# Kernel optimization log

Measured on AMD Instinct MI355X. Metric: run time of the kernel, lower is better.

Reference implementation:

```python
import jax, jax.numpy as jnp
import numpy as np

IN_FEATURES = 128
OUT_FEATURES = 128
GRID_SIZE = 5
SPLINE_ORDER = 3
N_KNOTS = GRID_SIZE + 2 * SPLINE_ORDER + 1  # 12
N_BASIS = GRID_SIZE + SPLINE_ORDER          # 8


def b_spline_basis(x, grid, spline_order):
    # x: [N, in], grid: [in, n_knots] -> basis: [N, in, n_basis]
    xe = x[..., None]
    basis = ((xe >= grid[..., :-1]) & (xe < grid[..., 1:])).astype(x.dtype)
    for k in range(1, spline_order + 1):
        left = (xe - grid[..., :-(k + 1)]) / (grid[..., k:-1] - grid[..., :-(k + 1)] + 1e-08)
        right = (grid[..., k + 1:] - xe) / (grid[..., k + 1:] - grid[..., 1:-k] + 1e-08)
        basis = left * basis[..., :-1] + right * basis[..., 1:]
    return basis


def setup_inputs() -> dict:
    key = jax.random.key(0)
    k_x, k_bw, k_sw = jax.random.split(key, 3)
    x = jax.random.normal(k_x, (16, 4096, IN_FEATURES), dtype=jnp.float32)
    grid = jnp.tile(jnp.linspace(-1.0, 1.0, N_KNOTS, dtype=jnp.float32)[None, :], (IN_FEATURES, 1))
    base_weight = jax.random.normal(k_bw, (OUT_FEATURES, IN_FEATURES), dtype=jnp.float32) * 0.1
    base_bias = jnp.zeros((OUT_FEATURES,), dtype=jnp.float32)
    spline_weight = jax.random.normal(k_sw, (OUT_FEATURES, IN_FEATURES, N_BASIS), dtype=jnp.float32) * 0.1
    spline_bias = jnp.zeros((OUT_FEATURES,), dtype=jnp.float32)
    spline_scale = jnp.ones((1,), dtype=jnp.float32)
    return {"x": x, "grid": grid, "base_weight": base_weight, "base_bias": base_bias,
            "spline_weight": spline_weight, "spline_bias": spline_bias, "spline_scale": spline_scale}


def reference(x, grid, base_weight, base_bias, spline_weight, spline_bias, spline_scale):
    orig_shape = x.shape
    x_flat = x.reshape(-1, IN_FEATURES)                      # [N, in]
    base_out = jax.nn.silu(x_flat) @ base_weight.T + base_bias  # [N, out]
    x_norm = jnp.tanh(x_flat)
    basis = b_spline_basis(x_norm, grid, SPLINE_ORDER)       # [N, in, n_basis]
    spline_out = jnp.einsum('oib,nib->no', spline_weight, basis) + spline_bias
    out = base_out + spline_scale * spline_out
    return out.reshape(*orig_shape[:-1], OUT_FEATURES)
```

## Files before the change

kernel.cpp:

```cpp
#include <hip/hip_runtime.h>
#include <hip/hip_bf16.h>


typedef __attribute__((ext_vector_type(8))) short short8;
typedef __attribute__((ext_vector_type(4))) float f32x4;
typedef __attribute__((ext_vector_type(4))) unsigned int u32x4;
typedef __attribute__((ext_vector_type(8))) unsigned short u16x8;

#define GLOAD_LDS16(g, l) __builtin_amdgcn_global_load_lds(                 \
    (const __attribute__((address_space(1))) void*)(g),                     \
    (__attribute__((address_space(3))) void*)(l), 16, 0, 0)

__device__ __forceinline__ unsigned short f2bf(float f) {
    unsigned u = __builtin_bit_cast(unsigned, f);
    return (unsigned short)((u + 0x7fffu + ((u >> 16) & 1u)) >> 16);
}
__device__ __forceinline__ unsigned pack_bf2(float lo, float hi) {
    unsigned r;
    asm("v_cvt_pk_bf16_f32 %0, %1, %2" : "=v"(r) : "v"(lo), "v"(hi));
    return r;
}
__device__ __forceinline__ float fexp2(float f) { return __builtin_amdgcn_exp2f(f); }
__device__ __forceinline__ float frcp(float f)  { return __builtin_amdgcn_rcpf(f); }
__device__ __forceinline__ float fsilu(float v) {
    return v * frcp(1.0f + fexp2(v * -1.442695041f));
}

__device__ __forceinline__ short8 spline_frag(float xv) {
    const float s6 = 0.16666667f;
    float e  = fexp2(xv * 2.885390082f);
    float r  = frcp(1.0f + e);
    float t  = __builtin_fmaf(-2.0f, r, 1.0f);
    float u  = __builtin_fmaf(t, 5.5f, 5.5f);
    int   j  = (int)u;
    float w  = u - (float)j;
    float w2 = w * w;
    float v0 = __builtin_fmaf(__builtin_fmaf(__builtin_fmaf(-s6, w, 0.5f), w, -0.5f), w, s6);
    float v1 = __builtin_fmaf(__builtin_fmaf(0.5f, w, -1.0f), w2, 0.66666667f);
    float v3 = (w * s6) * w2;
    float v2 = (1.0f - v0) - (v1 + v3);
    unsigned P01 = pack_bf2(v0, v1);
    unsigned P23 = pack_bf2(v2, v3);
    unsigned long long P = (unsigned long long)P01 | ((unsigned long long)P23 << 32);
    int s = (j - 3) << 4;
    unsigned long long lo, hi;
    lo = (s >= 0) ? ((s < 64) ? (P << s) : 0ull) : (P >> (-s));
    hi = (s <= 0) ? 0ull
                  : ((s < 64) ? (P >> (64 - s))
                              : ((s < 128) ? (P << (s - 64)) : 0ull));
    u32x4 f = { (unsigned)lo, (unsigned)(lo >> 32), (unsigned)hi, (unsigned)(hi >> 32) };
    return __builtin_bit_cast(short8, f);
}

__global__ void kan_prep(const float* __restrict__ spline_w,
                         const float* __restrict__ base_w,
                         const float* __restrict__ scale_p,
                         unsigned short* __restrict__ wpre) {
    int g   = blockIdx.x * 256 + threadIdx.x;
    int hp  = g >> 10;
    int rem = g & 1023;
    int o   = rem >> 3;
    int k0  = (rem & 7) << 3;
    const float* src = (hp < 16) ? (spline_w + (o << 10) + (hp << 6) + k0)
                                 : (base_w + (o << 7) + ((hp - 16) << 6) + k0);
    float s = (hp < 16) ? scale_p[0] : 1.0f;
    float4 a = *(const float4*)(src);
    float4 b = *(const float4*)(src + 4);
    u16x8 pk = { f2bf(a.x * s), f2bf(a.y * s), f2bf(a.z * s), f2bf(a.w * s),
                 f2bf(b.x * s), f2bf(b.y * s), f2bf(b.z * s), f2bf(b.w * s) };
    unsigned byte = (unsigned)(((o << 7) + (k0 << 1)) ^ ((o & 7) << 4));
    *(u16x8*)((char*)wpre + (hp << 14) + byte) = pk;
}

__global__ __launch_bounds__(128, 2) void kan_main(
    const float* __restrict__ x,
    const unsigned short* __restrict__ wpre,
    const float* __restrict__ base_b,
    const float* __restrict__ spline_b,
    const float* __restrict__ scale_p,
    float* __restrict__ out)
{
    __shared__ unsigned short lds_w[2 * 64 * 128];

    const int tid  = threadIdx.x;
    const int lane = tid & 63;
    const int wave = tid >> 6;
    const int l15  = lane & 15;
    const int kb   = lane >> 4;
    const int row0 = (int)blockIdx.x * 64;

    f32x4 acc[2][8];
#pragma unroll
    for (int m = 0; m < 2; ++m)
#pragma unroll
        for (int n = 0; n < 8; ++n) acc[m][n] = (f32x4){0.f, 0.f, 0.f, 0.f};

    char* lwbase = (char*)lds_w;
    const char* wsrc = (const char*)wpre;

    const float* xp0 = x + (row0 + (wave << 5) + l15) * 128 + kb;
    const float* xp1 = xp0 + 16 * 128;

    {
        const char* src = wsrc + (tid << 4);
        char* dst = lwbase + (tid << 4);
#pragma unroll
        for (int it = 0; it < 8; ++it)
            GLOAD_LDS16(src + (it << 11), dst + (it << 11));
    }
    float xsA[2][2], xsB[2][2];
    float4 xb0[2][2][2], xb1[2][2][2];
#pragma unroll
    for (int ks = 0; ks < 2; ++ks) {
        xsA[0][ks] = xp0[ks << 2];
        xsA[1][ks] = xp1[ks << 2];
    }
    __syncthreads();

#define STAGE(PN)                                                             \
    {                                                                         \
        const char* src = wsrc + ((PN) << 14) + (tid << 4);                   \
        char* dst = lwbase + (((PN) & 1) << 14) + (tid << 4);                 \
        _Pragma("unroll")                                                     \
        for (int it = 0; it < 8; ++it)                                        \
            GLOAD_LDS16(src + (it << 11), dst + (it << 11));                  \
    }

#define BREAD_MFMA(P_CUR, AF)                                                 \
    {                                                                         \
        char* cur = lwbase + (((P_CUR) & 1) << 14);                           \
        _Pragma("unroll")                                                     \
        for (int ks = 0; ks < 2; ++ks) {                                      \
            short8 bfr[8];                                                    \
            _Pragma("unroll")                                                 \
            for (int n = 0; n < 8; ++n) {                                     \
                int o = (n << 4) + l15;                                       \
                unsigned byte = (unsigned)(((o << 7) + (ks << 6) + (kb << 4)) \
                                           ^ ((o & 7) << 4));                 \
                bfr[n] = *(const short8*)(cur + byte);                        \
            }                                                                 \
            _Pragma("unroll")                                                 \
            for (int m = 0; m < 2; ++m)                                       \
                _Pragma("unroll")                                             \
                for (int n = 0; n < 8; ++n)                                   \
                    acc[m][n] = __builtin_amdgcn_mfma_f32_16x16x32_bf16(      \
                        AF[m][ks], bfr[n], acc[m][n], 0, 0, 0);               \
        }                                                                     \
    }

    for (int hp = 0; hp < 16; hp += 2) {
        {
            const int P = hp;
            STAGE(P + 1)
#pragma unroll
            for (int ks = 0; ks < 2; ++ks) {
                xsB[0][ks] = xp0[((P + 1) << 3) + (ks << 2)];
                xsB[1][ks] = xp1[((P + 1) << 3) + (ks << 2)];
            }
            short8 af[2][2];
#pragma unroll
            for (int m = 0; m < 2; ++m)
#pragma unroll
                for (int ks = 0; ks < 2; ++ks) af[m][ks] = spline_frag(xsA[m][ks]);
            BREAD_MFMA(P, af)
            __syncthreads();
        }
        {
            const int P = hp + 1;
            STAGE(P + 1)
            if (P < 15) {
#pragma unroll
                for (int ks = 0; ks < 2; ++ks) {
                    xsA[0][ks] = xp0[((P + 1) << 3) + (ks << 2)];
                    xsA[1][ks] = xp1[((P + 1) << 3) + (ks << 2)];
                }
            } else {
                const float* xq0 = x + (row0 + (wave << 5) + l15) * 128 + (kb << 3);
                const float* xq1 = xq0 + 16 * 128;
#pragma unroll
                for (int ks = 0; ks < 2; ++ks) {
                    xb0[0][ks][0] = *(const float4*)(xq0 + (ks << 5));
                    xb0[0][ks][1] = *(const float4*)(xq0 + (ks << 5) + 4);
                    xb0[1][ks][0] = *(const float4*)(xq1 + (ks << 5));
                    xb0[1][ks][1] = *(const float4*)(xq1 + (ks << 5) + 4);
                }
            }
            short8 af[2][2];
#pragma unroll
            for (int m = 0; m < 2; ++m)
#pragma unroll
                for (int ks = 0; ks < 2; ++ks) af[m][ks] = spline_frag(xsB[m][ks]);
            BREAD_MFMA(P, af)
            __syncthreads();
        }
    }

    {
        STAGE(17)
        const float* xq0 = x + (row0 + (wave << 5) + l15) * 128 + 64 + (kb << 3);
        const float* xq1 = xq0 + 16 * 128;
#pragma unroll
        for (int ks = 0; ks < 2; ++ks) {
            xb1[0][ks][0] = *(const float4*)(xq0 + (ks << 5));
            xb1[0][ks][1] = *(const float4*)(xq0 + (ks << 5) + 4);
            xb1[1][ks][0] = *(const float4*)(xq1 + (ks << 5));
            xb1[1][ks][1] = *(const float4*)(xq1 + (ks << 5) + 4);
        }
        short8 af[2][2];
#pragma unroll
        for (int m = 0; m < 2; ++m)
#pragma unroll
            for (int ks = 0; ks < 2; ++ks) {
                float4 a0 = xb0[m][ks][0], a1 = xb0[m][ks][1];
                u32x4 f = { pack_bf2(fsilu(a0.x), fsilu(a0.y)),
                            pack_bf2(fsilu(a0.z), fsilu(a0.w)),
                            pack_bf2(fsilu(a1.x), fsilu(a1.y)),
                            pack_bf2(fsilu(a1.z), fsilu(a1.w)) };
                af[m][ks] = __builtin_bit_cast(short8, f);
            }
        BREAD_MFMA(16, af)
        __syncthreads();
    }
    {
        short8 af[2][2];
#pragma unroll
        for (int m = 0; m < 2; ++m)
#pragma unroll
            for (int ks = 0; ks < 2; ++ks) {
                float4 a0 = xb1[m][ks][0], a1 = xb1[m][ks][1];
                u32x4 f = { pack_bf2(fsilu(a0.x), fsilu(a0.y)),
                            pack_bf2(fsilu(a0.z), fsilu(a0.w)),
                            pack_bf2(fsilu(a1.x), fsilu(a1.y)),
                            pack_bf2(fsilu(a1.z), fsilu(a1.w)) };
                af[m][ks] = __builtin_bit_cast(short8, f);
            }
        BREAD_MFMA(17, af)
    }
#undef BREAD_MFMA
#undef STAGE

    const float scale = scale_p[0];
    float* ob = out + (row0 + (wave << 5) + (kb << 2)) * 128 + l15;
#pragma unroll
    for (int n = 0; n < 8; ++n) {
        int o = (n << 4) + l15;
        float bias = base_b[o] + scale * spline_b[o];
#pragma unroll
        for (int m = 0; m < 2; ++m) {
            float* obm = ob + (m << 4) * 128 + (n << 4);
#pragma unroll
            for (int j = 0; j < 4; ++j)
                obm[j * 128] = acc[m][n][j] + bias;
        }
    }
}

extern "C" void kernel_launch(void* const* d_in, const int* in_sizes, int n_in,
                              void* d_out, int out_size, void* d_ws, size_t ws_size,
                              hipStream_t stream) {
    const float* x  = (const float*)d_in[0];
    const float* bw = (const float*)d_in[2];
    const float* bb = (const float*)d_in[3];
    const float* sw = (const float*)d_in[4];
    const float* sb = (const float*)d_in[5];
    const float* sc = (const float*)d_in[6];
    float* out = (float*)d_out;

    unsigned short* wpre = (unsigned short*)d_ws;
    hipLaunchKernelGGL(kan_prep, dim3(72), dim3(256), 0, stream, sw, bw, sc, wpre);

    int nrows   = in_sizes[0] / 128;
    int nblocks = nrows / 64;
    hipLaunchKernelGGL(kan_main, dim3(nblocks), dim3(128), 0, stream,
                       x, wpre, bb, sb, sc, out);
}
```

Measured before the change: 43.26 us.

## Double rows per block so each wave computes 64 rows

Each block now covers 128 rows instead of 64, with every wave owning 64 rows (four 16-row M tiles) instead of 32. Each bf16 weight slice staged into LDS is reused across twice as many rows, which halves total weight traffic and LDS fills per output row. The SiLU base-path inputs are now loaded right before use rather than prefetched a stage early. The cost is a doubled accumulator footprint (128 floats per lane) and half as many blocks (512), which may hurt occupancy under launch_bounds(128,2) and expose more load latency.

Measured after the change: 78.28 us. 81.0% more time.

```diff
diff --git a/kernel.cpp b/kernel.cpp
--- a/kernel.cpp
+++ b/kernel.cpp
@@ -64,10 +64,10 @@
     const float* src = (hp < 16) ? (spline_w + (o << 10) + (hp << 6) + k0)
                                  : (base_w + (o << 7) + ((hp - 16) << 6) + k0);
     float s = (hp < 16) ? scale_p[0] : 1.0f;
-    float4 a = *(const float4*)(src);
-    float4 b = *(const float4*)(src + 4);
-    u16x8 pk = { f2bf(a.x * s), f2bf(a.y * s), f2bf(a.z * s), f2bf(a.w * s),
-                 f2bf(b.x * s), f2bf(b.y * s), f2bf(b.z * s), f2bf(b.w * s) };
+    f32x4 a = *(const f32x4*)(src);
+    f32x4 b = *(const f32x4*)(src + 4);
+    u16x8 pk = { f2bf(a[0] * s), f2bf(a[1] * s), f2bf(a[2] * s), f2bf(a[3] * s),
+                 f2bf(b[0] * s), f2bf(b[1] * s), f2bf(b[2] * s), f2bf(b[3] * s) };
     unsigned byte = (unsigned)(((o << 7) + (k0 << 1)) ^ ((o & 7) << 4));
     *(u16x8*)((char*)wpre + (hp << 14) + byte) = pk;
 }
@@ -87,19 +87,18 @@
     const int wave = tid >> 6;
     const int l15  = lane & 15;
     const int kb   = lane >> 4;
-    const int row0 = (int)blockIdx.x * 64;
-
-    f32x4 acc[2][8];
-#pragma unroll
-    for (int m = 0; m < 2; ++m)
+    const int row0 = (int)blockIdx.x * 128 + (wave << 6);
+
+    f32x4 acc[4][8];
+#pragma unroll
+    for (int m = 0; m < 4; ++m)
 #pragma unroll
         for (int n = 0; n < 8; ++n) acc[m][n] = (f32x4){0.f, 0.f, 0.f, 0.f};
 
     char* lwbase = (char*)lds_w;
     const char* wsrc = (const char*)wpre;
 
-    const float* xp0 = x + (row0 + (wave << 5) + l15) * 128 + kb;
-    const float* xp1 = xp0 + 16 * 128;
+    const float* xp = x + (row0 + l15) * 128 + kb;
 
     {
         const char* src = wsrc + (tid << 4);
@@ -108,13 +107,12 @@
         for (int it = 0; it < 8; ++it)
             GLOAD_LDS16(src + (it << 11), dst + (it << 11));
     }
-    float xsA[2][2], xsB[2][2];
-    float4 xb0[2][2][2], xb1[2][2][2];
-#pragma unroll
-    for (int ks = 0; ks < 2; ++ks) {
-        xsA[0][ks] = xp0[ks << 2];
-        xsA[1][ks] = xp1[ks << 2];
-    }
+    float xsA[4][2], xsB[4][2];
+#pragma unroll
+    for (int m = 0; m < 4; ++m)
+#pragma unroll
+        for (int ks = 0; ks < 2; ++ks)
+            xsA[m][ks] = xp[m * 2048 + (ks << 2)];
     __syncthreads();
 
 #define STAGE(PN)                                                             \
@@ -140,7 +138,7 @@
                 bfr[n] = *(const short8*)(cur + byte);                        \
             }                                                                 \
             _Pragma("unroll")                                                 \
-            for (int m = 0; m < 2; ++m)                                       \
+            for (int m = 0; m < 4; ++m)                                       \
                 _Pragma("unroll")                                             \
                 for (int n = 0; n < 8; ++n)                                   \
                     acc[m][n] = __builtin_amdgcn_mfma_f32_16x16x32_bf16(      \
@@ -153,13 +151,13 @@
             const int P = hp;
             STAGE(P + 1)
 #pragma unroll
-            for (int ks = 0; ks < 2; ++ks) {
-                xsB[0][ks] = xp0[((P + 1) << 3) + (ks << 2)];
-                xsB[1][ks] = xp1[((P + 1) << 3) + (ks << 2)];
-            }
-            short8 af[2][2];
-#pragma unroll
-            for (int m = 0; m < 2; ++m)
+            for (int m = 0; m < 4; ++m)
+#pragma unroll
+                for (int ks = 0; ks < 2; ++ks)
+                    xsB[m][ks] = xp[m * 2048 + ((P + 1) << 3) + (ks << 2)];
+            short8 af[4][2];
+#pragma unroll
+            for (int m = 0; m < 4; ++m)
 #pragma unroll
                 for (int ks = 0; ks < 2; ++ks) af[m][ks] = spline_frag(xsA[m][ks]);
             BREAD_MFMA(P, af)
@@ -170,24 +168,14 @@
             STAGE(P + 1)
             if (P < 15) {
 #pragma unroll
-                for (int ks = 0; ks < 2; ++ks) {
-                    xsA[0][ks] = xp0[((P + 1) << 3) + (ks << 2)];
-                    xsA[1][ks] = xp1[((P + 1) << 3) + (ks << 2)];
-                }
-            } else {
-                const float* xq0 = x + (row0 + (wave << 5) + l15) * 128 + (kb << 3);
-                const float* xq1 = xq0 + 16 * 128;
-#pragma unroll
-                for (int ks = 0; ks < 2; ++ks) {
-                    xb0[0][ks][0] = *(const float4*)(xq0 + (ks << 5));
-                    xb0[0][ks][1] = *(const float4*)(xq0 + (ks << 5) + 4);
-                    xb0[1][ks][0] = *(const float4*)(xq1 + (ks << 5));
-                    xb0[1][ks][1] = *(const float4*)(xq1 + (ks << 5) + 4);
-                }
+                for (int m = 0; m < 4; ++m)
+#pragma unroll
+                    for (int ks = 0; ks < 2; ++ks)
+                        xsA[m][ks] = xp[m * 2048 + ((P + 1) << 3) + (ks << 2)];
             }
-            short8 af[2][2];
-#pragma unroll
-            for (int m = 0; m < 2; ++m)
+            short8 af[4][2];
+#pragma unroll
+            for (int m = 0; m < 4; ++m)
 #pragma unroll
                 for (int ks = 0; ks < 2; ++ks) af[m][ks] = spline_frag(xsB[m][ks]);
             BREAD_MFMA(P, af)
@@ -197,56 +185,53 @@
 
     {
         STAGE(17)
-        const float* xq0 = x + (row0 + (wave << 5) + l15) * 128 + 64 + (kb << 3);
-        const float* xq1 = xq0 + 16 * 128;
-#pragma unroll
-        for (int ks = 0; ks < 2; ++ks) {
-            xb1[0][ks][0] = *(const float4*)(xq0 + (ks << 5));
-            xb1[0][ks][1] = *(const float4*)(xq0 + (ks << 5) + 4);
-            xb1[1][ks][0] = *(const float4*)(xq1 + (ks << 5));
-            xb1[1][ks][1] = *(const float4*)(xq1 + (ks << 5) + 4);
-        }
-        short8 af[2][2];
-#pragma unroll
-        for (int m = 0; m < 2; ++m)
+        short8 af[4][2];
+#pragma unroll
+        for (int m = 0; m < 4; ++m) {
+            const float* xq = x + (row0 + (m << 4) + l15) * 128 + (kb << 3);
 #pragma unroll
             for (int ks = 0; ks < 2; ++ks) {
-                float4 a0 = xb0[m][ks][0], a1 = xb0[m][ks][1];
-                u32x4 f = { pack_bf2(fsilu(a0.x), fsilu(a0.y)),
-                            pack_bf2(fsilu(a0.z), fsilu(a0.w)),
-                            pack_bf2(fsilu(a1.x), fsilu(a1.y)),
-                            pack_bf2(fsilu(a1.z), fsilu(a1.w)) };
+                f32x4 p = *(const f32x4*)(xq + (ks << 5));
+                f32x4 q = *(const f32x4*)(xq + (ks << 5) + 4);
+                u32x4 f = { pack_bf2(fsilu(p[0]), fsilu(p[1])),
+                            pack_bf2(fsilu(p[2]), fsilu(p[3])),
+                            pack_bf2(fsilu(q[0]), fsilu(q[1])),
+                            pack_bf2(fsilu(q[2]), fsilu(q[3])) };
                 af[m][ks] = __builtin_bit_cast(short8, f);
             }
+        }
         BREAD_MFMA(16, af)
         __syncthreads();
     }
     {
-        short8 af[2][2];
-#pragma unroll
-        for (int m = 0; m < 2; ++m)
+        short8 af[4][2];
+#pragma unroll
+        for (int m = 0; m < 4; ++m) {
+            const float* xq = x + (row0 + (m << 4) + l15) * 128 + 64 + (kb << 3);
 #pragma unroll
             for (int ks = 0; ks < 2; ++ks) {
-                float4 a0 = xb1[m][ks][0], a1 = xb1[m][ks][1];
-                u32x4 f = { pack_bf2(fsilu(a0.x), fsilu(a0.y)),
-                            pack_bf2(fsilu(a0.z), fsilu(a0.w)),
-                            pack_bf2(fsilu(a1.x), fsilu(a1.y)),
-                            pack_bf2(fsilu(a1.z), fsilu(a1.w)) };
+                f32x4 p = *(const f32x4*)(xq + (ks << 5));
+                f32x4 q = *(const f32x4*)(xq + (ks << 5) + 4);
+                u32x4 f = { pack_bf2(fsilu(p[0]), fsilu(p[1])),
+                            pack_bf2(fsilu(p[2]), fsilu(p[3])),
+                            pack_bf2(fsilu(q[0]), fsilu(q[1])),
+                            pack_bf2(fsilu(q[2]), fsilu(q[3])) };
                 af[m][ks] = __builtin_bit_cast(short8, f);
             }
+        }
         BREAD_MFMA(17, af)
     }
 #undef BREAD_MFMA
 #undef STAGE
 
     const float scale = scale_p[0];
-    float* ob = out + (row0 + (wave << 5) + (kb << 2)) * 128 + l15;
+    float* ob = out + (row0 + (kb << 2)) * 128 + l15;
 #pragma unroll
     for (int n = 0; n < 8; ++n) {
         int o = (n << 4) + l15;
         float bias = base_b[o] + scale * spline_b[o];
 #pragma unroll
-        for (int m = 0; m < 2; ++m) {
+        for (int m = 0; m < 4; ++m) {
             float* obm = ob + (m << 4) * 128 + (n << 4);
 #pragma unroll
             for (int j = 0; j < 4; ++j)
@@ -270,7 +255,7 @@
     hipLaunchKernelGGL(kan_prep, dim3(72), dim3(256), 0, stream, sw, bw, sc, wpre);
 
     int nrows   = in_sizes[0] / 128;
-    int nblocks = nrows / 64;
+    int nblocks = nrows / 128;
     hipLaunchKernelGGL(kan_main, dim3(nblocks), dim3(128), 0, stream,
                        x, wpre, bb, sb, sc, out);
 }
```

## Triple-buffer weight panels in LDS with partial vmcnt waits and MFMA priority

Applied to the files above, without the earlier changes.

Moves the LDS weight staging from a double buffer to a triple buffer, prefetching two panels ahead. Full __syncthreads are replaced with explicit s_waitcnt vmcnt(N) plus s_barrier, so in-flight global-to-LDS loads for later panels can stay outstanding across the barrier. MFMA sections are wrapped in s_setprio to favour the compute wave. The cost is extra LDS per block (48KB), which may limit occupancy. Correctness depends on the hand-counted vmcnt values matching the actual issued load order.

New measurement: 63.46 us. 1.47x slower.

```diff
diff --git a/kernel.cpp b/kernel.cpp
--- a/kernel.cpp
+++ b/kernel.cpp
@@ -10,6 +10,12 @@
 #define GLOAD_LDS16(g, l) __builtin_amdgcn_global_load_lds(                 \
     (const __attribute__((address_space(1))) void*)(g),                     \
     (__attribute__((address_space(3))) void*)(l), 16, 0, 0)
+
+#define PIPE_BAR(NSTR) do {                                                 \
+    asm volatile("s_waitcnt vmcnt(" NSTR ") lgkmcnt(0)" ::: "memory");      \
+    __builtin_amdgcn_s_barrier();                                           \
+    __builtin_amdgcn_sched_barrier(0);                                      \
+} while (0)
 
 __device__ __forceinline__ unsigned short f2bf(float f) {
     unsigned u = __builtin_bit_cast(unsigned, f);
@@ -64,10 +70,10 @@
     const float* src = (hp < 16) ? (spline_w + (o << 10) + (hp << 6) + k0)
                                  : (base_w + (o << 7) + ((hp - 16) << 6) + k0);
     float s = (hp < 16) ? scale_p[0] : 1.0f;
-    float4 a = *(const float4*)(src);
-    float4 b = *(const float4*)(src + 4);
-    u16x8 pk = { f2bf(a.x * s), f2bf(a.y * s), f2bf(a.z * s), f2bf(a.w * s),
-                 f2bf(b.x * s), f2bf(b.y * s), f2bf(b.z * s), f2bf(b.w * s) };
+    f32x4 a = *(const f32x4*)(src);
+    f32x4 b = *(const f32x4*)(src + 4);
+    u16x8 pk = { f2bf(a[0] * s), f2bf(a[1] * s), f2bf(a[2] * s), f2bf(a[3] * s),
+                 f2bf(b[0] * s), f2bf(b[1] * s), f2bf(b[2] * s), f2bf(b[3] * s) };
     unsigned byte = (unsigned)(((o << 7) + (k0 << 1)) ^ ((o & 7) << 4));
     *(u16x8*)((char*)wpre + (hp << 14) + byte) = pk;
 }
@@ -80,7 +86,7 @@
     const float* __restrict__ scale_p,
     float* __restrict__ out)
 {
-    __shared__ unsigned short lds_w[2 * 64 * 128];
+    __shared__ unsigned short lds_w[3 * 64 * 128];
 
     const int tid  = threadIdx.x;
     const int lane = tid & 63;
@@ -101,26 +107,10 @@
     const float* xp0 = x + (row0 + (wave << 5) + l15) * 128 + kb;
     const float* xp1 = xp0 + 16 * 128;
 
-    {
-        const char* src = wsrc + (tid << 4);
-        char* dst = lwbase + (tid << 4);
-#pragma unroll
-        for (int it = 0; it < 8; ++it)
-            GLOAD_LDS16(src + (it << 11), dst + (it << 11));
-    }
-    float xsA[2][2], xsB[2][2];
-    float4 xb0[2][2][2], xb1[2][2][2];
-#pragma unroll
-    for (int ks = 0; ks < 2; ++ks) {
-        xsA[0][ks] = xp0[ks << 2];
-        xsA[1][ks] = xp1[ks << 2];
-    }
-    __syncthreads();
-
 #define STAGE(PN)                                                             \
     {                                                                         \
         const char* src = wsrc + ((PN) << 14) + (tid << 4);                   \
-        char* dst = lwbase + (((PN) & 1) << 14) + (tid << 4);                 \
+        char* dst = lwbase + ((PN) % 3) * 16384 + (tid << 4);                 \
         _Pragma("unroll")                                                     \
         for (int it = 0; it < 8; ++it)                                        \
             GLOAD_LDS16(src + (it << 11), dst + (it << 11));                  \
@@ -128,7 +118,8 @@
 
 #define BREAD_MFMA(P_CUR, AF)                                                 \
     {                                                                         \
-        char* cur = lwbase + (((P_CUR) & 1) << 14);                           \
+        char* cur = lwbase + ((P_CUR) % 3) * 16384;                           \
+        __builtin_amdgcn_s_setprio(1);                                        \
         _Pragma("unroll")                                                     \
         for (int ks = 0; ks < 2; ++ks) {                                      \
             short8 bfr[8];                                                    \
@@ -146,12 +137,25 @@
                     acc[m][n] = __builtin_amdgcn_mfma_f32_16x16x32_bf16(      \
                         AF[m][ks], bfr[n], acc[m][n], 0, 0, 0);               \
         }                                                                     \
-    }
-
-    for (int hp = 0; hp < 16; hp += 2) {
+        __builtin_amdgcn_s_setprio(0);                                        \
+    }
+
+    float xsA[2][2], xsB[2][2];
+    float4 xb0[2][2][2], xb1[2][2][2];
+
+    STAGE(0)
+    STAGE(1)
+#pragma unroll
+    for (int ks = 0; ks < 2; ++ks) {
+        xsA[0][ks] = xp0[ks << 2];
+        xsA[1][ks] = xp1[ks << 2];
+    }
+    PIPE_BAR("12");
+
+    for (int hp = 0; hp < 14; hp += 2) {
         {
             const int P = hp;
-            STAGE(P + 1)
+            STAGE(P + 2)
 #pragma unroll
             for (int ks = 0; ks < 2; ++ks) {
                 xsB[0][ks] = xp0[((P + 1) << 3) + (ks << 2)];
@@ -163,27 +167,15 @@
 #pragma unroll
                 for (int ks = 0; ks < 2; ++ks) af[m][ks] = spline_frag(xsA[m][ks]);
             BREAD_MFMA(P, af)
-            __syncthreads();
+            PIPE_BAR("12");
         }
         {
             const int P = hp + 1;
-            STAGE(P + 1)
-            if (P < 15) {
-#pragma unroll
-                for (int ks = 0; ks < 2; ++ks) {
-                    xsA[0][ks] = xp0[((P + 1) << 3) + (ks << 2)];
-                    xsA[1][ks] = xp1[((P + 1) << 3) + (ks << 2)];
-                }
-            } else {
-                const float* xq0 = x + (row0 + (wave << 5) + l15) * 128 + (kb << 3);
-                const float* xq1 = xq0 + 16 * 128;
-#pragma unroll
-                for (int ks = 0; ks < 2; ++ks) {
-                    xb0[0][ks][0] = *(const float4*)(xq0 + (ks << 5));
-                    xb0[0][ks][1] = *(const float4*)(xq0 + (ks << 5) + 4);
-                    xb0[1][ks][0] = *(const float4*)(xq1 + (ks << 5));
-                    xb0[1][ks][1] = *(const float4*)(xq1 + (ks << 5) + 4);
-                }
+            STAGE(P + 2)
+#pragma unroll
+            for (int ks = 0; ks < 2; ++ks) {
+                xsA[0][ks] = xp0[((P + 1) << 3) + (ks << 2)];
+                xsA[1][ks] = xp1[((P + 1) << 3) + (ks << 2)];
             }
             short8 af[2][2];
 #pragma unroll
@@ -191,12 +183,45 @@
 #pragma unroll
                 for (int ks = 0; ks < 2; ++ks) af[m][ks] = spline_frag(xsB[m][ks]);
             BREAD_MFMA(P, af)
-            __syncthreads();
-        }
-    }
-
+            PIPE_BAR("12");
+        }
+    }
+
+    {
+        STAGE(16)
+#pragma unroll
+        for (int ks = 0; ks < 2; ++ks) {
+            xsB[0][ks] = xp0[(15 << 3) + (ks << 2)];
+            xsB[1][ks] = xp1[(15 << 3) + (ks << 2)];
+        }
+        short8 af[2][2];
+#pragma unroll
+        for (int m = 0; m < 2; ++m)
+#pragma unroll
+            for (int ks = 0; ks < 2; ++ks) af[m][ks] = spline_frag(xsA[m][ks]);
+        BREAD_MFMA(14, af)
+        PIPE_BAR("12");
+    }
     {
         STAGE(17)
+        const float* xq0 = x + (row0 + (wave << 5) + l15) * 128 + (kb << 3);
+        const float* xq1 = xq0 + 16 * 128;
+#pragma unroll
+        for (int ks = 0; ks < 2; ++ks) {
+            xb0[0][ks][0] = *(const float4*)(xq0 + (ks << 5));
+            xb0[0][ks][1] = *(const float4*)(xq0 + (ks << 5) + 4);
+            xb0[1][ks][0] = *(const float4*)(xq1 + (ks << 5));
+            xb0[1][ks][1] = *(const float4*)(xq1 + (ks << 5) + 4);
+        }
+        short8 af[2][2];
+#pragma unroll
+        for (int m = 0; m < 2; ++m)
+#pragma unroll
+            for (int ks = 0; ks < 2; ++ks) af[m][ks] = spline_frag(xsB[m][ks]);
+        BREAD_MFMA(15, af)
+        PIPE_BAR("16");
+    }
+    {
         const float* xq0 = x + (row0 + (wave << 5) + l15) * 128 + 64 + (kb << 3);
         const float* xq1 = xq0 + 16 * 128;
 #pragma unroll
@@ -219,7 +244,7 @@
                 af[m][ks] = __builtin_bit_cast(short8, f);
             }
         BREAD_MFMA(16, af)
-        __syncthreads();
+        PIPE_BAR("8");
     }
     {
         short8 af[2][2];
```
